# Kernel optimization log

Hardware: AMD Instinct MI355X
Metric: run time of the kernel (lower is better)

The kernel has to match this reference:

```python
import jax, jax.numpy as jnp
import numpy as np

FL = 48  # featurelength


def _sage(x, src, dst, Wl, bl, Wr):
    # PyG SAGEConv (mean aggr): lin_l(mean_{j in N(i)} x_j) + lin_r(x_i); bias on lin_l.
    N = x.shape[0]
    agg = jax.ops.segment_sum(x[src], dst, num_segments=N)
    cnt = jax.ops.segment_sum(jnp.ones((src.shape[0], 1), x.dtype), dst, num_segments=N)
    mean = agg / jnp.maximum(cnt, 1.0)
    return mean @ Wl + bl + x @ Wr


def _pool2(x, H):
    # x: (H*H, C) node features on an HxH grid -> 2x2 max pool -> (H/2*H/2, C)
    C = x.shape[1]
    xc = x.T.reshape(C, H // 2, 2, H // 2, 2)
    return xc.max(axis=(2, 4)).reshape(C, (H // 2) * (H // 2)).T


def _att_block(x, src, dst, am_W, am_b, ax_W, ax_b, c_Wl, c_bl, c_Wr):
    # spatial attention: sigmoid(fc(mean) + fc(max)) over nodes, per-channel gate
    att = jax.nn.sigmoid(jnp.mean(x, 0)[None] @ am_W + am_b + jnp.max(x, 0)[None] @ ax_W + ax_b)
    # channel attention: SAGEConv -> (N,1) gate broadcast over channels
    ch = jax.nn.sigmoid(_sage(x, src, dst, c_Wl, c_bl, c_Wr))
    return x + x * att + x * ch


def setup_inputs() -> dict:
    key = jax.random.key(0)
    ks = iter(jax.random.split(key, 64))
    d = {}
    d['x_image'] = jax.random.normal(next(ks), (128, 128), jnp.float32)
    sizes = [(16384, 65536), (4096, 16384), (1024, 4096), (256, 1024)]
    for i, (n, e) in enumerate(sizes):
        d[f'e{i}'] = jax.random.randint(next(ks), (2, e), 0, n)
    d['train'] = 0

    def lin(kin, kout, k):
        s = 1.0 / np.sqrt(kin)
        return jax.random.uniform(k, (kin, kout), jnp.float32, -s, s)

    # gconv1..4 (in: 1,48,48,48 -> out 48)
    for i, cin in enumerate([1, FL, FL, FL], start=1):
        d[f'g{i}_Wl'] = lin(cin, FL, next(ks))
        d[f'g{i}_bl'] = jnp.zeros((FL,), jnp.float32)
        d[f'g{i}_Wr'] = lin(cin, FL, next(ks))
    # attention blocks 1..4
    for i in range(1, 5):
        d[f'am{i}_W'] = lin(FL, FL, next(ks)); d[f'am{i}_b'] = jnp.zeros((FL,), jnp.float32)
        d[f'ax{i}_W'] = lin(FL, FL, next(ks)); d[f'ax{i}_b'] = jnp.zeros((FL,), jnp.float32)
        d[f'c{i}_Wl'] = lin(FL, 1, next(ks)); d[f'c{i}_bl'] = jnp.zeros((1,), jnp.float32)
        d[f'c{i}_Wr'] = lin(FL, 1, next(ks))
    d['fc1_W'] = lin(FL * 16 * 16, 256, next(ks)); d['fc1_b'] = jnp.zeros((256,), jnp.float32)
    d['fc2_W'] = lin(256, 10, next(ks)); d['fc2_b'] = jnp.zeros((10,), jnp.float32)
    return d


def reference(x_image,
              g1_Wl, g1_bl, g1_Wr, g2_Wl, g2_bl, g2_Wr,
              g3_Wl, g3_bl, g3_Wr, g4_Wl, g4_bl, g4_Wr,
              am1_W, am1_b, ax1_W, ax1_b, c1_Wl, c1_bl, c1_Wr,
              am2_W, am2_b, ax2_W, ax2_b, c2_Wl, c2_bl, c2_Wr,
              am3_W, am3_b, ax3_W, ax3_b, c3_Wl, c3_bl, c3_Wr,
              am4_W, am4_b, ax4_W, ax4_b, c4_Wl, c4_bl, c4_Wr,
              fc1_W, fc1_b, fc2_W, fc2_b,
              e0, e1, e2, e3, train):
    x = x_image.reshape(128 * 128, 1)  # (16384, 1) node features
    # level 1: SAGE on 128x128 graph, pool to 64x64, attention on 64x64 graph (e1)
    x = jax.nn.relu(_sage(x, e0[0], e0[1], g1_Wl, g1_bl, g1_Wr))
    x = _pool2(x, 128)
    x = _att_block(x, e1[0], e1[1], am1_W, am1_b, ax1_W, ax1_b, c1_Wl, c1_bl, c1_Wr)
    # level 2
    x = jax.nn.relu(_sage(x, e1[0], e1[1], g2_Wl, g2_bl, g2_Wr))
    x = _pool2(x, 64)
    x = _att_block(x, e2[0], e2[1], am2_W, am2_b, ax2_W, ax2_b, c2_Wl, c2_bl, c2_Wr)
    # level 3
    x = jax.nn.relu(_sage(x, e2[0], e2[1], g3_Wl, g3_bl, g3_Wr))
    x = _pool2(x, 32)
    x = _att_block(x, e3[0], e3[1], am3_W, am3_b, ax3_W, ax3_b, c3_Wl, c3_bl, c3_Wr)
    # level 4 (no pool; flatten channels-major like torch transpose+reshape)
    x = jax.nn.relu(_sage(x, e3[0], e3[1], g4_Wl, g4_bl, g4_Wr))  # (256, 48)
    x = x.T.reshape(1, FL * 16 * 16)
    x = jax.nn.relu(x @ fc1_W + fc1_b)
    logits = x @ fc2_W + fc2_b
    return jax.nn.log_softmax(logits, axis=1)
```

## Files before the change

### kernel.cpp

```cpp
#include <hip/hip_runtime.h>
#include <math.h>

#define FL 48

__device__ __forceinline__ float sigmoidf(float v) { return 1.0f / (1.0f + expf(-v)); }


__global__ void k_zero(float* __restrict__ p, int n) {
  int i = blockIdx.x * blockDim.x + threadIdx.x;
  if (i < n) p[i] = 0.0f;
}

__global__ __launch_bounds__(256) void k_prep(
    const int* __restrict__ e0, const int* __restrict__ e1,
    const int* __restrict__ e2, const int* __restrict__ e3,
    const float* __restrict__ ximg,
    float* __restrict__ cnt0, float* __restrict__ cnt1,
    float* __restrict__ cnt2, float* __restrict__ cnt3,
    float* __restrict__ aggS0) {
  int g = blockIdx.x * 256 + threadIdx.x;
  if (g < 65536) {
    int d = e0[65536 + g];
    atomicAdd(&cnt0[d], 1.0f);
    atomicAdd(&aggS0[d], ximg[e0[g]]);
  } else if (g < 65536 + 16384) {
    atomicAdd(&cnt1[e1[16384 + (g - 65536)]], 1.0f);
  } else if (g < 65536 + 16384 + 4096) {
    atomicAdd(&cnt2[e2[4096 + (g - 81920)]], 1.0f);
  } else if (g < 65536 + 16384 + 4096 + 1024) {
    atomicAdd(&cnt3[e3[1024 + (g - 86016)]], 1.0f);
  }
}

__global__ __launch_bounds__(256) void k_sage1pool(
    const float* __restrict__ x, const float* __restrict__ agg, const float* __restrict__ cnt,
    const float* __restrict__ Wl, const float* __restrict__ bl, const float* __restrict__ Wr,
    float* __restrict__ y) {
  int g = blockIdx.x * 256 + threadIdx.x;
  if (g >= 4096 * FL) return;
  int c = g % FL, m = g / FL;
  int a = m >> 6, b = m & 63;
  float wl = Wl[c], wr = Wr[c], bb = bl[c];
  float best = -INFINITY;
#pragma unroll
  for (int da = 0; da < 2; ++da)
#pragma unroll
    for (int db = 0; db < 2; ++db) {
      int n = (2 * a + da) * 128 + (2 * b + db);
      float mean = agg[n] / fmaxf(cnt[n], 1.0f);
      float v = fmaxf(mean * wl + bb + x[n] * wr, 0.0f);
      best = fmaxf(best, v);
    }
  y[g] = best;
}

__global__ __launch_bounds__(256) void k_a(
    const float* __restrict__ x, int N,
    const float* __restrict__ cWl, const float* __restrict__ cWr,
    float* __restrict__ mean_out, float* __restrict__ max_out,
    float* __restrict__ dl, float* __restrict__ dr) {
  if (blockIdx.x < FL) {
    int c = blockIdx.x, t = threadIdx.x;
    float s = 0.0f, m = -INFINITY;
    for (int n = t; n < N; n += 256) {
      float v = x[n * FL + c];
      s += v; m = fmaxf(m, v);
    }
    __shared__ float ss[256], sm[256];
    ss[t] = s; sm[t] = m;
    __syncthreads();
    for (int o = 128; o > 0; o >>= 1) {
      if (t < o) { ss[t] += ss[t + o]; sm[t] = fmaxf(sm[t], sm[t + o]); }
      __syncthreads();
    }
    if (t == 0) { mean_out[c] = ss[0] / (float)N; max_out[c] = sm[0]; }
  } else {
    int n = (blockIdx.x - FL) * 256 + threadIdx.x;
    if (n >= N) return;
    float a = 0.0f, b = 0.0f;
    const float* xr = x + n * FL;
    for (int c = 0; c < FL; ++c) { float v = xr[c]; a += v * cWl[c]; b += v * cWr[c]; }
    dl[n] = a; dr[n] = b;
  }
}

__global__ __launch_bounds__(256) void k_b(
    const float* __restrict__ mean, const float* __restrict__ mx,
    const float* __restrict__ amW, const float* __restrict__ amb,
    const float* __restrict__ axW, const float* __restrict__ axb,
    float* __restrict__ att,
    const int* __restrict__ e, int E, const float* __restrict__ dl,
    float* __restrict__ aggS) {
  if (blockIdx.x == 0) {
    int co = threadIdx.x;
    if (co < FL) {
      float s = amb[co] + axb[co];
      for (int ci = 0; ci < FL; ++ci)
        s += mean[ci] * amW[ci * FL + co] + mx[ci] * axW[ci * FL + co];
      att[co] = sigmoidf(s);
    }
  } else {
    int i = (blockIdx.x - 1) * 256 + threadIdx.x;
    if (i < E) atomicAdd(&aggS[e[E + i]], dl[e[i]]);
  }
}

__global__ __launch_bounds__(256) void k_c(
    const int* __restrict__ e, int E,
    const float* __restrict__ x, const float* __restrict__ att,
    const float* __restrict__ aggS, const float* __restrict__ cnt,
    const float* __restrict__ dr, const float* __restrict__ cbl,
    float* __restrict__ aggC) {
  int g = blockIdx.x * 256 + threadIdx.x;
  if (g >= E * FL) return;
  int ei = g / FL, c = g % FL;
  int s = e[ei], d = e[E + ei];
  float ch = sigmoidf(aggS[s] / fmaxf(cnt[s], 1.0f) + cbl[0] + dr[s]);
  float v = x[s * FL + c] * (1.0f + att[c] + ch);
  atomicAdd(&aggC[d * FL + c], v);
}

template <int POOL>
__global__ __launch_bounds__(256) void k_d(
    const float* __restrict__ x, const float* __restrict__ aggC, const float* __restrict__ cnt,
    const float* __restrict__ aggS, const float* __restrict__ dr,
    const float* __restrict__ att, const float* __restrict__ cbl,
    const float* __restrict__ Wl, const float* __restrict__ blv, const float* __restrict__ Wr,
    float* __restrict__ y, int H, int Nout) {
  __shared__ float sWl[FL * FL], sWr[FL * FL], sAtt[FL];
  for (int i = threadIdx.x; i < FL * FL; i += 256) { sWl[i] = Wl[i]; sWr[i] = Wr[i]; }
  if (threadIdx.x < FL) sAtt[threadIdx.x] = att[threadIdx.x];
  __syncthreads();
  int g = blockIdx.x * 256 + threadIdx.x;
  if (g >= Nout * FL) return;
  int c = g % FL, m = g / FL;
  float result;
  if (POOL) {
    int Ho = H >> 1;
    int a = m / Ho, b = m % Ho;
    float best = -INFINITY;
#pragma unroll
    for (int da = 0; da < 2; ++da)
#pragma unroll
      for (int db = 0; db < 2; ++db) {
        int n = (2 * a + da) * H + (2 * b + db);
        float rc = 1.0f / fmaxf(cnt[n], 1.0f);
        float ch = sigmoidf(aggS[n] * rc + cbl[0] + dr[n]);
        const float* xr = x + n * FL;
        const float* ar = aggC + n * FL;
        float s = blv[c];
        for (int ci = 0; ci < FL; ++ci)
          s += ar[ci] * rc * sWl[ci * FL + c] + xr[ci] * (1.0f + sAtt[ci] + ch) * sWr[ci * FL + c];
        best = fmaxf(best, fmaxf(s, 0.0f));
      }
    result = best;
  } else {
    int n = m;
    float rc = 1.0f / fmaxf(cnt[n], 1.0f);
    float ch = sigmoidf(aggS[n] * rc + cbl[0] + dr[n]);
    const float* xr = x + n * FL;
    const float* ar = aggC + n * FL;
    float s = blv[c];
    for (int ci = 0; ci < FL; ++ci)
      s += ar[ci] * rc * sWl[ci * FL + c] + xr[ci] * (1.0f + sAtt[ci] + ch) * sWr[ci * FL + c];
    result = fmaxf(s, 0.0f);
  }
  y[g] = result;
}

__global__ __launch_bounds__(256) void k_fc1(const float* __restrict__ x4,
                                             const float* __restrict__ W,
                                             float* __restrict__ acc) {
  __shared__ float xin[128];
  int b = blockIdx.x, t = threadIdx.x;
  int k0 = b * 128;
  if (t < 128) {
    int k = k0 + t;
    int c = k >> 8, n = k & 255;
    xin[t] = x4[n * FL + c];
  }
  __syncthreads();
  float a = 0.0f;
  for (int i = 0; i < 128; ++i) a += xin[i] * W[(size_t)(k0 + i) * 256 + t];
  atomicAdd(&acc[t], a);
}

__global__ void k_fc_final(const float* __restrict__ acc, const float* __restrict__ b1,
                           const float* __restrict__ W2, const float* __restrict__ b2,
                           float* __restrict__ out) {
  __shared__ float a[256];
  __shared__ float logits[10];
  int t = threadIdx.x;
  a[t] = fmaxf(acc[t] + b1[t], 0.0f);
  __syncthreads();
  if (t < 10) {
    float s = b2[t];
    for (int o = 0; o < 256; ++o) s += a[o] * W2[o * 10 + t];
    logits[t] = s;
  }
  __syncthreads();
  if (t == 0) {
    float m = logits[0];
    for (int j = 1; j < 10; ++j) m = fmaxf(m, logits[j]);
    float s = 0.0f;
    for (int j = 0; j < 10; ++j) s += expf(logits[j] - m);
    float ls = logf(s);
    for (int j = 0; j < 10; ++j) out[j] = logits[j] - m - ls;
  }
}


static inline int cdiv(int a, int b) { return (a + b - 1) / b; }

extern "C" void kernel_launch(void* const* d_in, const int* in_sizes, int n_in,
                              void* d_out, int out_size, void* d_ws, size_t ws_size,
                              hipStream_t stream) {
  const float* x_image = (const float*)d_in[0];
  const int* e0 = (const int*)d_in[1];
  const int* e1 = (const int*)d_in[2];
  const int* e2 = (const int*)d_in[3];
  const int* e3 = (const int*)d_in[4];
  const float* g1_Wl = (const float*)d_in[6];
  const float* g1_bl = (const float*)d_in[7];
  const float* g1_Wr = (const float*)d_in[8];
  const float* gWl[3] = {(const float*)d_in[9], (const float*)d_in[12], (const float*)d_in[15]};
  const float* gbl[3] = {(const float*)d_in[10], (const float*)d_in[13], (const float*)d_in[16]};
  const float* gWr[3] = {(const float*)d_in[11], (const float*)d_in[14], (const float*)d_in[17]};
  const float* amW[3]; const float* amb[3]; const float* axW[3]; const float* axb[3];
  const float* cWl[3]; const float* cbl[3]; const float* cWr[3];
  for (int i = 0; i < 3; ++i) {
    int base = 18 + i * 7;
    amW[i] = (const float*)d_in[base + 0];
    amb[i] = (const float*)d_in[base + 1];
    axW[i] = (const float*)d_in[base + 2];
    axb[i] = (const float*)d_in[base + 3];
    cWl[i] = (const float*)d_in[base + 4];
    cbl[i] = (const float*)d_in[base + 5];
    cWr[i] = (const float*)d_in[base + 6];
  }
  const float* fc1_W = (const float*)d_in[46];
  const float* fc1_b = (const float*)d_in[47];
  const float* fc2_W = (const float*)d_in[48];
  const float* fc2_b = (const float*)d_in[49];
  float* out = (float*)d_out;

  const int N0 = 16384, E1v = 16384;
  const int N1 = 4096, E2v = 4096;
  const int N2 = 1024, E3v = 1024;
  const int N3 = 256;

  float* f = (float*)d_ws;
  float* xp1 = f;
  float* xp2 = xp1 + N1 * FL;
  float* xp3 = xp2 + N2 * FL;
  float* x4  = xp3 + N3 * FL;
  float* dl  = x4 + N3 * FL;
  float* dr  = dl + N1;
  float* stats = dr + N1;
  float* zbase = stats + 144;
  float* cnt0 = zbase;
  float* cnt1 = cnt0 + N0;
  float* cnt2 = cnt1 + N1;
  float* cnt3 = cnt2 + N2;
  float* aggS0 = cnt3 + N3;
  float* aggS1 = aggS0 + N0;
  float* aggS2 = aggS1 + N1;
  float* aggS3 = aggS2 + N2;
  float* aggC2 = aggS3 + N3;
  float* aggC3 = aggC2 + N1 * FL;
  float* aggC4 = aggC3 + N2 * FL;
  float* fc1acc = aggC4 + N3 * FL;
  int zcount = (int)((fc1acc + 256) - zbase);

  float* mean = stats;
  float* mx = stats + 48;
  float* att = stats + 96;

  k_zero<<<cdiv(zcount, 256), 256, 0, stream>>>(zbase, zcount);
  k_prep<<<cdiv(87040, 256), 256, 0, stream>>>(e0, e1, e2, e3, x_image,
                                               cnt0, cnt1, cnt2, cnt3, aggS0);
  k_sage1pool<<<cdiv(N1 * FL, 256), 256, 0, stream>>>(x_image, aggS0, cnt0,
                                                      g1_Wl, g1_bl, g1_Wr, xp1);

  k_a<<<FL + cdiv(N1, 256), 256, 0, stream>>>(xp1, N1, cWl[0], cWr[0], mean, mx, dl, dr);
  k_b<<<1 + cdiv(E1v, 256), 256, 0, stream>>>(mean, mx, amW[0], amb[0], axW[0], axb[0], att,
                                              e1, E1v, dl, aggS1);
  k_c<<<cdiv(E1v * FL, 256), 256, 0, stream>>>(e1, E1v, xp1, att, aggS1, cnt1, dr, cbl[0], aggC2);
  k_d<1><<<cdiv(N2 * FL, 256), 256, 0, stream>>>(xp1, aggC2, cnt1, aggS1, dr, att, cbl[0],
                                                 gWl[0], gbl[0], gWr[0], xp2, 64, N2);

  k_a<<<FL + cdiv(N2, 256), 256, 0, stream>>>(xp2, N2, cWl[1], cWr[1], mean, mx, dl, dr);
  k_b<<<1 + cdiv(E2v, 256), 256, 0, stream>>>(mean, mx, amW[1], amb[1], axW[1], axb[1], att,
                                              e2, E2v, dl, aggS2);
  k_c<<<cdiv(E2v * FL, 256), 256, 0, stream>>>(e2, E2v, xp2, att, aggS2, cnt2, dr, cbl[1], aggC3);
  k_d<1><<<cdiv(N3 * FL, 256), 256, 0, stream>>>(xp2, aggC3, cnt2, aggS2, dr, att, cbl[1],
                                                 gWl[1], gbl[1], gWr[1], xp3, 32, N3);

  k_a<<<FL + cdiv(N3, 256), 256, 0, stream>>>(xp3, N3, cWl[2], cWr[2], mean, mx, dl, dr);
  k_b<<<1 + cdiv(E3v, 256), 256, 0, stream>>>(mean, mx, amW[2], amb[2], axW[2], axb[2], att,
                                              e3, E3v, dl, aggS3);
  k_c<<<cdiv(E3v * FL, 256), 256, 0, stream>>>(e3, E3v, xp3, att, aggS3, cnt3, dr, cbl[2], aggC4);
  k_d<0><<<cdiv(N3 * FL, 256), 256, 0, stream>>>(xp3, aggC4, cnt3, aggS3, dr, att, cbl[2],
                                                 gWl[2], gbl[2], gWr[2], x4, 16, N3);

  k_fc1<<<96, 256, 0, stream>>>(x4, fc1_W, fc1acc);
  k_fc_final<<<1, 256, 0, stream>>>(fc1acc, fc1_b, fc2_W, fc2_b, out);

  (void)in_sizes; (void)n_in; (void)out_size; (void)ws_size;
}
```

Before: 96.24 us.

## Fuse attention statistics and channel projections into producer kernels via atomics

Folds the per-channel mean/max reductions and the dl/dr channel-attention projections into the kernels that produce each level's features, using LDS atomics and global atomics. The attention-gate MLP is now recomputed per block inside the scatter and SAGE kernels, so the separate k_a and k_b launches go away. The zero kernel becomes a hipMemsetAsync, and fc1 is split into 128 blocks of 96 rows instead of 96 blocks of 128. This cuts several dependent launches per level, at the cost of heavy per-element atomics on dl/dr and redundant per-block attention-gate work. The float atomicMax-as-unsigned trick is only valid because the values are non-negative after ReLU.

After: 190.8 us. 98.3% more time.

```diff
diff --git a/kernel.cpp b/kernel.cpp
--- a/kernel.cpp
+++ b/kernel.cpp
@@ -5,11 +5,18 @@
 
 __device__ __forceinline__ float sigmoidf(float v) { return 1.0f / (1.0f + expf(-v)); }
 
-
-__global__ void k_zero(float* __restrict__ p, int n) {
-  int i = blockIdx.x * blockDim.x + threadIdx.x;
-  if (i < n) p[i] = 0.0f;
-}
+__device__ __forceinline__ void att_lds(const float* sum, const float* mxv, float invN,
+                                        const float* amW, const float* amb,
+                                        const float* axW, const float* axb, float* sAtt) {
+  int t = threadIdx.x;
+  if (t < FL) {
+    float s = amb[t] + axb[t];
+    for (int ci = 0; ci < FL; ++ci)
+      s += (sum[ci] * invN) * amW[ci * FL + t] + mxv[ci] * axW[ci * FL + t];
+    sAtt[t] = sigmoidf(s);
+  }
+}
+
 
 __global__ __launch_bounds__(256) void k_prep(
     const int* __restrict__ e0, const int* __restrict__ e1,
@@ -23,179 +30,180 @@
     int d = e0[65536 + g];
     atomicAdd(&cnt0[d], 1.0f);
     atomicAdd(&aggS0[d], ximg[e0[g]]);
-  } else if (g < 65536 + 16384) {
+  } else if (g < 81920) {
     atomicAdd(&cnt1[e1[16384 + (g - 65536)]], 1.0f);
-  } else if (g < 65536 + 16384 + 4096) {
+  } else if (g < 86016) {
     atomicAdd(&cnt2[e2[4096 + (g - 81920)]], 1.0f);
-  } else if (g < 65536 + 16384 + 4096 + 1024) {
+  } else if (g < 87040) {
     atomicAdd(&cnt3[e3[1024 + (g - 86016)]], 1.0f);
   }
 }
 
-__global__ __launch_bounds__(256) void k_sage1pool(
+__global__ __launch_bounds__(256) void k_p2(
     const float* __restrict__ x, const float* __restrict__ agg, const float* __restrict__ cnt,
     const float* __restrict__ Wl, const float* __restrict__ bl, const float* __restrict__ Wr,
-    float* __restrict__ y) {
+    const float* __restrict__ cWl, const float* __restrict__ cWr,
+    float* __restrict__ y, float* __restrict__ sum1, float* __restrict__ max1,
+    float* __restrict__ dl, float* __restrict__ dr) {
+  __shared__ float lsum[FL];
+  __shared__ unsigned lmax[FL];
+  if (threadIdx.x < FL) { lsum[threadIdx.x] = 0.0f; lmax[threadIdx.x] = 0u; }
+  __syncthreads();
   int g = blockIdx.x * 256 + threadIdx.x;
-  if (g >= 4096 * FL) return;
-  int c = g % FL, m = g / FL;
-  int a = m >> 6, b = m & 63;
-  float wl = Wl[c], wr = Wr[c], bb = bl[c];
-  float best = -INFINITY;
+  if (g < 4096 * FL) {
+    int c = g % FL, m = g / FL;
+    int a = m >> 6, b = m & 63;
+    float wl = Wl[c], wr = Wr[c], bb = bl[c];
+    float best = -INFINITY;
 #pragma unroll
-  for (int da = 0; da < 2; ++da)
+    for (int da = 0; da < 2; ++da)
 #pragma unroll
-    for (int db = 0; db < 2; ++db) {
-      int n = (2 * a + da) * 128 + (2 * b + db);
-      float mean = agg[n] / fmaxf(cnt[n], 1.0f);
-      float v = fmaxf(mean * wl + bb + x[n] * wr, 0.0f);
-      best = fmaxf(best, v);
-    }
-  y[g] = best;
-}
-
-__global__ __launch_bounds__(256) void k_a(
-    const float* __restrict__ x, int N,
-    const float* __restrict__ cWl, const float* __restrict__ cWr,
-    float* __restrict__ mean_out, float* __restrict__ max_out,
-    float* __restrict__ dl, float* __restrict__ dr) {
-  if (blockIdx.x < FL) {
-    int c = blockIdx.x, t = threadIdx.x;
-    float s = 0.0f, m = -INFINITY;
-    for (int n = t; n < N; n += 256) {
-      float v = x[n * FL + c];
-      s += v; m = fmaxf(m, v);
-    }
-    __shared__ float ss[256], sm[256];
-    ss[t] = s; sm[t] = m;
-    __syncthreads();
-    for (int o = 128; o > 0; o >>= 1) {
-      if (t < o) { ss[t] += ss[t + o]; sm[t] = fmaxf(sm[t], sm[t + o]); }
-      __syncthreads();
-    }
-    if (t == 0) { mean_out[c] = ss[0] / (float)N; max_out[c] = sm[0]; }
-  } else {
-    int n = (blockIdx.x - FL) * 256 + threadIdx.x;
-    if (n >= N) return;
-    float a = 0.0f, b = 0.0f;
-    const float* xr = x + n * FL;
-    for (int c = 0; c < FL; ++c) { float v = xr[c]; a += v * cWl[c]; b += v * cWr[c]; }
-    dl[n] = a; dr[n] = b;
-  }
-}
-
-__global__ __launch_bounds__(256) void k_b(
-    const float* __restrict__ mean, const float* __restrict__ mx,
+      for (int db = 0; db < 2; ++db) {
+        int n = (2 * a + da) * 128 + (2 * b + db);
+        float mean = agg[n] / fmaxf(cnt[n], 1.0f);
+        best = fmaxf(best, fmaxf(mean * wl + bb + x[n] * wr, 0.0f));
+      }
+    y[g] = best;
+    atomicAdd(&lsum[c], best);
+    atomicMax(&lmax[c], __float_as_uint(best));
+    atomicAdd(&dl[m], best * cWl[c]);
+    atomicAdd(&dr[m], best * cWr[c]);
+  }
+  __syncthreads();
+  if (threadIdx.x < FL) {
+    atomicAdd(&sum1[threadIdx.x], lsum[threadIdx.x]);
+    atomicMax((unsigned*)&max1[threadIdx.x], lmax[threadIdx.x]);
+  }
+}
+
+__global__ __launch_bounds__(256) void k_edge(const int* __restrict__ e, int E,
+                                              const float* __restrict__ dl,
+                                              float* __restrict__ aggS) {
+  int i = blockIdx.x * 256 + threadIdx.x;
+  if (i < E) atomicAdd(&aggS[e[E + i]], dl[e[i]]);
+}
+
+__global__ __launch_bounds__(256) void k_gscat(
+    const int* __restrict__ e, int E, int N,
+    const float* __restrict__ x,
+    const float* __restrict__ sum, const float* __restrict__ mxv,
     const float* __restrict__ amW, const float* __restrict__ amb,
     const float* __restrict__ axW, const float* __restrict__ axb,
-    float* __restrict__ att,
-    const int* __restrict__ e, int E, const float* __restrict__ dl,
-    float* __restrict__ aggS) {
-  if (blockIdx.x == 0) {
-    int co = threadIdx.x;
-    if (co < FL) {
-      float s = amb[co] + axb[co];
-      for (int ci = 0; ci < FL; ++ci)
-        s += mean[ci] * amW[ci * FL + co] + mx[ci] * axW[ci * FL + co];
-      att[co] = sigmoidf(s);
-    }
-  } else {
-    int i = (blockIdx.x - 1) * 256 + threadIdx.x;
-    if (i < E) atomicAdd(&aggS[e[E + i]], dl[e[i]]);
-  }
-}
-
-__global__ __launch_bounds__(256) void k_c(
-    const int* __restrict__ e, int E,
-    const float* __restrict__ x, const float* __restrict__ att,
     const float* __restrict__ aggS, const float* __restrict__ cnt,
     const float* __restrict__ dr, const float* __restrict__ cbl,
     float* __restrict__ aggC) {
+  __shared__ float sAtt[FL];
+  att_lds(sum, mxv, 1.0f / (float)N, amW, amb, axW, axb, sAtt);
+  __syncthreads();
   int g = blockIdx.x * 256 + threadIdx.x;
   if (g >= E * FL) return;
   int ei = g / FL, c = g % FL;
   int s = e[ei], d = e[E + ei];
   float ch = sigmoidf(aggS[s] / fmaxf(cnt[s], 1.0f) + cbl[0] + dr[s]);
-  float v = x[s * FL + c] * (1.0f + att[c] + ch);
-  atomicAdd(&aggC[d * FL + c], v);
-}
-
-template <int POOL>
-__global__ __launch_bounds__(256) void k_d(
-    const float* __restrict__ x, const float* __restrict__ aggC, const float* __restrict__ cnt,
-    const float* __restrict__ aggS, const float* __restrict__ dr,
-    const float* __restrict__ att, const float* __restrict__ cbl,
-    const float* __restrict__ Wl, const float* __restrict__ blv, const float* __restrict__ Wr,
-    float* __restrict__ y, int H, int Nout) {
+  atomicAdd(&aggC[d * FL + c], x[s * FL + c] * (1.0f + sAtt[c] + ch));
+}
+
+template <int POOL, int HAS_NEXT>
+__global__ __launch_bounds__(256) void k_gsage(
+    const float* __restrict__ x, int N, int H, int Nout,
+    const float* __restrict__ sum, const float* __restrict__ mxv,
+    const float* __restrict__ amW, const float* __restrict__ amb,
+    const float* __restrict__ axW, const float* __restrict__ axb,
+    const float* __restrict__ aggS, const float* __restrict__ cnt,
+    const float* __restrict__ dr, const float* __restrict__ cbl,
+    const float* __restrict__ aggC,
+    const float* __restrict__ Wl, const float* __restrict__ bl,
+    const float* __restrict__ Wr,
+    float* __restrict__ y,
+    float* __restrict__ nsum, float* __restrict__ nmax,
+    float* __restrict__ ndl, float* __restrict__ ndr,
+    const float* __restrict__ ncWl, const float* __restrict__ ncWr) {
   __shared__ float sWl[FL * FL], sWr[FL * FL], sAtt[FL];
+  __shared__ float lsum[FL];
+  __shared__ unsigned lmax[FL];
+  att_lds(sum, mxv, 1.0f / (float)N, amW, amb, axW, axb, sAtt);
   for (int i = threadIdx.x; i < FL * FL; i += 256) { sWl[i] = Wl[i]; sWr[i] = Wr[i]; }
-  if (threadIdx.x < FL) sAtt[threadIdx.x] = att[threadIdx.x];
+  if (HAS_NEXT && threadIdx.x < FL) { lsum[threadIdx.x] = 0.0f; lmax[threadIdx.x] = 0u; }
   __syncthreads();
   int g = blockIdx.x * 256 + threadIdx.x;
-  if (g >= Nout * FL) return;
-  int c = g % FL, m = g / FL;
-  float result;
-  if (POOL) {
-    int Ho = H >> 1;
-    int a = m / Ho, b = m % Ho;
-    float best = -INFINITY;
+  float cb = cbl[0];
+  if (g < Nout * FL) {
+    int c = g % FL, m = g / FL;
+    float result;
+    if (POOL) {
+      int Ho = H >> 1;
+      int a = m / Ho, b = m % Ho;
+      float best = -INFINITY;
 #pragma unroll
-    for (int da = 0; da < 2; ++da)
+      for (int da = 0; da < 2; ++da)
 #pragma unroll
-      for (int db = 0; db < 2; ++db) {
-        int n = (2 * a + da) * H + (2 * b + db);
-        float rc = 1.0f / fmaxf(cnt[n], 1.0f);
-        float ch = sigmoidf(aggS[n] * rc + cbl[0] + dr[n]);
-        const float* xr = x + n * FL;
-        const float* ar = aggC + n * FL;
-        float s = blv[c];
-        for (int ci = 0; ci < FL; ++ci)
-          s += ar[ci] * rc * sWl[ci * FL + c] + xr[ci] * (1.0f + sAtt[ci] + ch) * sWr[ci * FL + c];
-        best = fmaxf(best, fmaxf(s, 0.0f));
-      }
-    result = best;
-  } else {
-    int n = m;
-    float rc = 1.0f / fmaxf(cnt[n], 1.0f);
-    float ch = sigmoidf(aggS[n] * rc + cbl[0] + dr[n]);
-    const float* xr = x + n * FL;
-    const float* ar = aggC + n * FL;
-    float s = blv[c];
-    for (int ci = 0; ci < FL; ++ci)
-      s += ar[ci] * rc * sWl[ci * FL + c] + xr[ci] * (1.0f + sAtt[ci] + ch) * sWr[ci * FL + c];
-    result = fmaxf(s, 0.0f);
-  }
-  y[g] = result;
+        for (int db = 0; db < 2; ++db) {
+          int n = (2 * a + da) * H + (2 * b + db);
+          float rc = 1.0f / fmaxf(cnt[n], 1.0f);
+          float ch = sigmoidf(aggS[n] * rc + cb + dr[n]);
+          const float* xr = x + n * FL;
+          const float* ar = aggC + n * FL;
+          float s = bl[c];
+          for (int ci = 0; ci < FL; ++ci)
+            s += ar[ci] * rc * sWl[ci * FL + c] +
+                 xr[ci] * (1.0f + sAtt[ci] + ch) * sWr[ci * FL + c];
+          best = fmaxf(best, fmaxf(s, 0.0f));
+        }
+      result = best;
+    } else {
+      int n = m;
+      float rc = 1.0f / fmaxf(cnt[n], 1.0f);
+      float ch = sigmoidf(aggS[n] * rc + cb + dr[n]);
+      const float* xr = x + n * FL;
+      const float* ar = aggC + n * FL;
+      float s = bl[c];
+      for (int ci = 0; ci < FL; ++ci)
+        s += ar[ci] * rc * sWl[ci * FL + c] +
+             xr[ci] * (1.0f + sAtt[ci] + ch) * sWr[ci * FL + c];
+      result = fmaxf(s, 0.0f);
+    }
+    y[g] = result;
+    if (HAS_NEXT) {
+      atomicAdd(&lsum[c], result);
+      atomicMax(&lmax[c], __float_as_uint(result));
+      atomicAdd(&ndl[m], result * ncWl[c]);
+      atomicAdd(&ndr[m], result * ncWr[c]);
+    }
+  }
+  __syncthreads();
+  if (HAS_NEXT && threadIdx.x < FL) {
+    atomicAdd(&nsum[threadIdx.x], lsum[threadIdx.x]);
+    atomicMax((unsigned*)&nmax[threadIdx.x], lmax[threadIdx.x]);
+  }
 }
 
 __global__ __launch_bounds__(256) void k_fc1(const float* __restrict__ x4,
                                              const float* __restrict__ W,
                                              float* __restrict__ acc) {
-  __shared__ float xin[128];
-  int b = blockIdx.x, t = threadIdx.x;
-  int k0 = b * 128;
-  if (t < 128) {
+  __shared__ float xin[96];
+  int k0 = blockIdx.x * 96;
+  int t = threadIdx.x;
+  if (t < 96) {
     int k = k0 + t;
-    int c = k >> 8, n = k & 255;
-    xin[t] = x4[n * FL + c];
+    xin[t] = x4[(k & 255) * FL + (k >> 8)];
   }
   __syncthreads();
   float a = 0.0f;
-  for (int i = 0; i < 128; ++i) a += xin[i] * W[(size_t)(k0 + i) * 256 + t];
+  for (int i = 0; i < 96; ++i) a += xin[i] * W[(size_t)(k0 + i) * 256 + t];
   atomicAdd(&acc[t], a);
 }
 
-__global__ void k_fc_final(const float* __restrict__ acc, const float* __restrict__ b1,
-                           const float* __restrict__ W2, const float* __restrict__ b2,
-                           float* __restrict__ out) {
-  __shared__ float a[256];
+__global__ void k_final(const float* __restrict__ acc, const float* __restrict__ b1,
+                        const float* __restrict__ W2, const float* __restrict__ b2,
+                        float* __restrict__ out) {
+  __shared__ float av[256];
   __shared__ float logits[10];
   int t = threadIdx.x;
-  a[t] = fmaxf(acc[t] + b1[t], 0.0f);
+  av[t] = fmaxf(acc[t] + b1[t], 0.0f);
   __syncthreads();
   if (t < 10) {
     float s = b2[t];
-    for (int o = 0; o < 256; ++o) s += a[o] * W2[o * 10 + t];
+    for (int o = 0; o < 256; ++o) s += av[o] * W2[o * 10 + t];
     logits[t] = s;
   }
   __syncthreads();
@@ -215,14 +223,13 @@
 extern "C" void kernel_launch(void* const* d_in, const int* in_sizes, int n_in,
                               void* d_out, int out_size, void* d_ws, size_t ws_size,
                               hipStream_t stream) {
-  const float* x_image = (const float*)d_in[0];
-  const int* e0 = (const int*)d_in[1];
-  const int* e1 = (const int*)d_in[2];
-  const int* e2 = (const int*)d_in[3];
-  const int* e3 = (const int*)d_in[4];
-  const float* g1_Wl = (const float*)d_in[6];
-  const float* g1_bl = (const float*)d_in[7];
-  const float* g1_Wr = (const float*)d_in[8];
+  const float* ximg = (const float*)d_in[0];
+  const int* e1v = (const int*)d_in[2];
+  const int* e2v = (const int*)d_in[3];
+  const int* e3v = (const int*)d_in[4];
+  const float* g1Wl = (const float*)d_in[6];
+  const float* g1bl = (const float*)d_in[7];
+  const float* g1Wr = (const float*)d_in[8];
   const float* gWl[3] = {(const float*)d_in[9], (const float*)d_in[12], (const float*)d_in[15]};
   const float* gbl[3] = {(const float*)d_in[10], (const float*)d_in[13], (const float*)d_in[16]};
   const float* gWr[3] = {(const float*)d_in[11], (const float*)d_in[14], (const float*)d_in[17]};
@@ -238,73 +245,83 @@
     cbl[i] = (const float*)d_in[base + 5];
     cWr[i] = (const float*)d_in[base + 6];
   }
-  const float* fc1_W = (const float*)d_in[46];
-  const float* fc1_b = (const float*)d_in[47];
-  const float* fc2_W = (const float*)d_in[48];
-  const float* fc2_b = (const float*)d_in[49];
+  const float* fc1W = (const float*)d_in[46];
+  const float* fc1b = (const float*)d_in[47];
+  const float* fc2W = (const float*)d_in[48];
+  const float* fc2b = (const float*)d_in[49];
   float* out = (float*)d_out;
 
-  const int N0 = 16384, E1v = 16384;
-  const int N1 = 4096, E2v = 4096;
-  const int N2 = 1024, E3v = 1024;
-  const int N3 = 256;
-
-  float* f = (float*)d_ws;
-  float* xp1 = f;
-  float* xp2 = xp1 + N1 * FL;
-  float* xp3 = xp2 + N2 * FL;
-  float* x4  = xp3 + N3 * FL;
-  float* dl  = x4 + N3 * FL;
-  float* dr  = dl + N1;
-  float* stats = dr + N1;
-  float* zbase = stats + 144;
-  float* cnt0 = zbase;
-  float* cnt1 = cnt0 + N0;
-  float* cnt2 = cnt1 + N1;
-  float* cnt3 = cnt2 + N2;
-  float* aggS0 = cnt3 + N3;
-  float* aggS1 = aggS0 + N0;
-  float* aggS2 = aggS1 + N1;
-  float* aggS3 = aggS2 + N2;
-  float* aggC2 = aggS3 + N3;
-  float* aggC3 = aggC2 + N1 * FL;
-  float* aggC4 = aggC3 + N2 * FL;
-  float* fc1acc = aggC4 + N3 * FL;
-  int zcount = (int)((fc1acc + 256) - zbase);
-
-  float* mean = stats;
-  float* mx = stats + 48;
-  float* att = stats + 96;
-
-  k_zero<<<cdiv(zcount, 256), 256, 0, stream>>>(zbase, zcount);
-  k_prep<<<cdiv(87040, 256), 256, 0, stream>>>(e0, e1, e2, e3, x_image,
+  const int N0 = 16384, N1 = 4096, N2 = 1024, N3 = 256;
+  const int E0 = 65536, E1 = 16384, E2 = 4096, E3 = 1024;
+
+  float* base = (float*)d_ws;
+  size_t off = 0;
+  auto alloc = [&](size_t n) -> float* {
+    float* q = base + off;
+    off += (n + 1023) & ~(size_t)1023;
+    return q;
+  };
+  float* cnt0 = alloc(N0);
+  float* cnt1 = alloc(N1);
+  float* cnt2 = alloc(N2);
+  float* cnt3 = alloc(N3);
+  float* aggS0 = alloc(N0);
+  float* aggS1 = alloc(N1);
+  float* aggS2 = alloc(N2);
+  float* aggS3 = alloc(N3);
+  float* aggC2 = alloc(N1 * FL);
+  float* aggC3 = alloc(N2 * FL);
+  float* aggC4 = alloc(N3 * FL);
+  float* sum1 = alloc(FL); float* max1 = alloc(FL);
+  float* sum2 = alloc(FL); float* max2 = alloc(FL);
+  float* sum3 = alloc(FL); float* max3 = alloc(FL);
+  float* dl2 = alloc(N1); float* dr2 = alloc(N1);
+  float* dl3 = alloc(N2); float* dr3 = alloc(N2);
+  float* dl4 = alloc(N3); float* dr4 = alloc(N3);
+  float* fc1acc = alloc(256);
+  size_t zbytes = off * sizeof(float);
+  float* xp1 = alloc(N1 * FL);
+  float* xp2 = alloc(N2 * FL);
+  float* xp3 = alloc(N3 * FL);
+  float* x4 = alloc(N3 * FL);
+
+  hipMemsetAsync(d_ws, 0, zbytes, stream);
+
+  k_prep<<<cdiv(87040, 256), 256, 0, stream>>>((const int*)d_in[1], e1v, e2v, e3v, ximg,
                                                cnt0, cnt1, cnt2, cnt3, aggS0);
-  k_sage1pool<<<cdiv(N1 * FL, 256), 256, 0, stream>>>(x_image, aggS0, cnt0,
-                                                      g1_Wl, g1_bl, g1_Wr, xp1);
-
-  k_a<<<FL + cdiv(N1, 256), 256, 0, stream>>>(xp1, N1, cWl[0], cWr[0], mean, mx, dl, dr);
-  k_b<<<1 + cdiv(E1v, 256), 256, 0, stream>>>(mean, mx, amW[0], amb[0], axW[0], axb[0], att,
-                                              e1, E1v, dl, aggS1);
-  k_c<<<cdiv(E1v * FL, 256), 256, 0, stream>>>(e1, E1v, xp1, att, aggS1, cnt1, dr, cbl[0], aggC2);
-  k_d<1><<<cdiv(N2 * FL, 256), 256, 0, stream>>>(xp1, aggC2, cnt1, aggS1, dr, att, cbl[0],
-                                                 gWl[0], gbl[0], gWr[0], xp2, 64, N2);
-
-  k_a<<<FL + cdiv(N2, 256), 256, 0, stream>>>(xp2, N2, cWl[1], cWr[1], mean, mx, dl, dr);
-  k_b<<<1 + cdiv(E2v, 256), 256, 0, stream>>>(mean, mx, amW[1], amb[1], axW[1], axb[1], att,
-                                              e2, E2v, dl, aggS2);
-  k_c<<<cdiv(E2v * FL, 256), 256, 0, stream>>>(e2, E2v, xp2, att, aggS2, cnt2, dr, cbl[1], aggC3);
-  k_d<1><<<cdiv(N3 * FL, 256), 256, 0, stream>>>(xp2, aggC3, cnt2, aggS2, dr, att, cbl[1],
-                                                 gWl[1], gbl[1], gWr[1], xp3, 32, N3);
-
-  k_a<<<FL + cdiv(N3, 256), 256, 0, stream>>>(xp3, N3, cWl[2], cWr[2], mean, mx, dl, dr);
-  k_b<<<1 + cdiv(E3v, 256), 256, 0, stream>>>(mean, mx, amW[2], amb[2], axW[2], axb[2], att,
-                                              e3, E3v, dl, aggS3);
-  k_c<<<cdiv(E3v * FL, 256), 256, 0, stream>>>(e3, E3v, xp3, att, aggS3, cnt3, dr, cbl[2], aggC4);
-  k_d<0><<<cdiv(N3 * FL, 256), 256, 0, stream>>>(xp3, aggC4, cnt3, aggS3, dr, att, cbl[2],
-                                                 gWl[2], gbl[2], gWr[2], x4, 16, N3);
-
-  k_fc1<<<96, 256, 0, stream>>>(x4, fc1_W, fc1acc);
-  k_fc_final<<<1, 256, 0, stream>>>(fc1acc, fc1_b, fc2_W, fc2_b, out);
+  k_p2<<<cdiv(N1 * FL, 256), 256, 0, stream>>>(ximg, aggS0, cnt0, g1Wl, g1bl, g1Wr,
+                                               cWl[0], cWr[0], xp1, sum1, max1, dl2, dr2);
+
+  k_edge<<<cdiv(E1, 256), 256, 0, stream>>>(e1v, E1, dl2, aggS1);
+  k_gscat<<<cdiv(E1 * FL, 256), 256, 0, stream>>>(e1v, E1, N1, xp1, sum1, max1,
+                                                  amW[0], amb[0], axW[0], axb[0],
+                                                  aggS1, cnt1, dr2, cbl[0], aggC2);
+  k_gsage<1, 1><<<cdiv(N2 * FL, 256), 256, 0, stream>>>(
+      xp1, N1, 64, N2, sum1, max1, amW[0], amb[0], axW[0], axb[0],
+      aggS1, cnt1, dr2, cbl[0], aggC2, gWl[0], gbl[0], gWr[0],
+      xp2, sum2, max2, dl3, dr3, cWl[1], cWr[1]);
+
+  k_edge<<<cdiv(E2, 256), 256, 0, stream>>>(e2v, E2, dl3, aggS2);
+  k_gscat<<<cdiv(E2 * FL, 256), 256, 0, stream>>>(e2v, E2, N2, xp2, sum2, max2,
+                                                  amW[1], amb[1], axW[1], axb[1],
+                                                  aggS2, cnt2, dr3, cbl[1], aggC3);
+  k_gsage<1, 1><<<cdiv(N3 * FL, 256), 256, 0, stream>>>(
+      xp2, N2, 32, N3, sum2, max2, amW[1], amb[1], axW[1], axb[1],
+      aggS2, cnt2, dr3, cbl[1], aggC3, gWl[1], gbl[1], gWr[1],
+      xp3, sum3, max3, dl4, dr4, cWl[2], cWr[2]);
+
+  k_edge<<<cdiv(E3, 256), 256, 0, stream>>>(e3v, E3, dl4, aggS3);
+  k_gscat<<<cdiv(E3 * FL, 256), 256, 0, stream>>>(e3v, E3, N3, xp3, sum3, max3,
+                                                  amW[2], amb[2], axW[2], axb[2],
+                                                  aggS3, cnt3, dr4, cbl[2], aggC4);
+  k_gsage<0, 0><<<cdiv(N3 * FL, 256), 256, 0, stream>>>(
+      xp3, N3, 16, N3, sum3, max3, amW[2], amb[2], axW[2], axb[2],
+      aggS3, cnt3, dr4, cbl[2], aggC4, gWl[2], gbl[2], gWr[2],
+      x4, (float*)nullptr, (float*)nullptr, (float*)nullptr, (float*)nullptr,
+      (const float*)nullptr, (const float*)nullptr);
+
+  k_fc1<<<128, 256, 0, stream>>>(x4, fc1W, fc1acc);
+  k_final<<<1, 256, 0, stream>>>(fc1acc, fc1b, fc2W, fc2b, out);
 
   (void)in_sizes; (void)n_in; (void)out_size; (void)ws_size;
 }
```
